# Performance work log

Measured on AMD Instinct MI355X. Metric: run time of the kernel, lower is better.

## Reference

```python
import jax, jax.numpy as jnp
import numpy as np

B, T, N_EMBD, HEAD_SIZE = 64, 512, 384, 64


def setup_inputs() -> dict:
    key = jax.random.key(0)
    k1, k2, k3, k4 = jax.random.split(key, 4)
    x = jax.random.normal(k1, (B, T, N_EMBD), dtype=jnp.float32)
    scale = 1.0 / np.sqrt(N_EMBD)
    Wq = jax.random.normal(k2, (N_EMBD, HEAD_SIZE), dtype=jnp.float32) * scale
    Wk = jax.random.normal(k3, (N_EMBD, HEAD_SIZE), dtype=jnp.float32) * scale
    Wv = jax.random.normal(k4, (N_EMBD, HEAD_SIZE), dtype=jnp.float32) * scale
    return {"x": x, "Wq": Wq, "Wk": Wk, "Wv": Wv}


def reference(x, Wq, Wk, Wv):
    # Single-head causal self-attention (dropout = identity / eval mode).
    q = jnp.einsum('btc,ch->bth', x, Wq)  # [B,T,H]
    k = jnp.einsum('btc,ch->bth', x, Wk)
    v = jnp.einsum('btc,ch->bth', x, Wv)
    scale = q.shape[-1] ** -0.5
    scores = jnp.einsum('bth,bsh->bts', q, k) * scale  # [B,T,T]
    Tlen = x.shape[1]
    causal = jnp.tril(jnp.ones((Tlen, Tlen), dtype=bool))
    scores = jnp.where(causal, scores, -jnp.inf)
    weights = jax.nn.softmax(scores, axis=-1)
    out = jnp.einsum('bts,bsh->bth', weights, v)  # [B,T,H]
    return out
```

## Files before the change

kernel.cpp:

```cpp
#include <hip/hip_runtime.h>


typedef __bf16 bf16_t;
typedef __bf16 bf16x8 __attribute__((ext_vector_type(8)));
typedef __bf16 bf16x4 __attribute__((ext_vector_type(4)));
typedef float  f32x4  __attribute__((ext_vector_type(4)));

__device__ __forceinline__ bf16x8 ld_b128(const bf16_t* p) {
    return *reinterpret_cast<const bf16x8*>(p);
}

__device__ __forceinline__ void async_copy16(void* lds, const void* g) {
    __builtin_amdgcn_global_load_lds(
        (const __attribute__((address_space(1))) unsigned int*)g,
        (__attribute__((address_space(3))) unsigned int*)lds,
        16, 0, 0);
}

__global__ __launch_bounds__(256) void wt_kernel(const float* __restrict__ Wq,
                                                 const float* __restrict__ Wk,
                                                 const float* __restrict__ Wv,
                                                 bf16_t* __restrict__ Wt) {
    int idx = blockIdx.x * 256 + threadIdx.x;
    int p = idx / (384 * 64);
    int r = idx - p * (384 * 64);
    int c = r >> 6;
    int h = r & 63;
    const float* W = (p == 0) ? Wq : (p == 1) ? Wk : Wv;
    Wt[p * 24576 + h * 384 + c] = (bf16_t)W[c * 64 + h];
}

__global__ __launch_bounds__(256, 2) void qkv_kernel(const float* __restrict__ x,
                                                     const bf16_t* __restrict__ Wt,
                                                     bf16_t* __restrict__ Q,
                                                     bf16_t* __restrict__ K,
                                                     bf16_t* __restrict__ Vt) {
    const int tid  = threadIdx.x;
    const int wave = tid >> 6, lane = tid & 63;
    const int quad = lane >> 4, l16 = lane & 15;
    const int rowbase = blockIdx.x * 64;
    const int batch   = rowbase >> 9;

    __shared__ alignas(16) float xs[2][64 * 128];

    bf16x8 Bf[3][12];
    #pragma unroll
    for (int nt = 0; nt < 3; ++nt) {
        int col  = wave * 48 + nt * 16 + l16;
        int proj = col >> 6, h = col & 63;
        const bf16_t* wp = Wt + proj * 24576 + h * 384 + quad * 8;
        #pragma unroll
        for (int kk = 0; kk < 12; ++kk) Bf[nt][kk] = ld_b128(wp + kk * 32);
    }

    auto stage = [&](int buf, int c) {
        const float* src = x + rowbase * 384 + c * 128;
        #pragma unroll
        for (int i = 0; i < 8; ++i) {
            int g   = wave * 512 + i * 64 + lane;
            int row = g >> 5, gc = g & 31;
            int gs  = (gc & 24) | ((gc ^ row) & 7);
            async_copy16(&xs[buf][(wave * 512 + i * 64) * 4],
                         src + row * 384 + gs * 4);
        }
    };

    f32x4 acc[4][3];
    #pragma unroll
    for (int rt = 0; rt < 4; ++rt)
        #pragma unroll
        for (int nt = 0; nt < 3; ++nt) acc[rt][nt] = (f32x4){0.f, 0.f, 0.f, 0.f};

    stage(0, 0);
    for (int c = 0; c < 3; ++c) {
        int buf = c & 1;
        __syncthreads();
        if (c < 2) stage(1 - buf, c + 1);
        #pragma unroll
        for (int rt = 0; rt < 4; ++rt) {
            int row = rt * 16 + l16;
            const float* xr = &xs[buf][row * 128];
            #pragma unroll
            for (int kk = 0; kk < 4; ++kk) {
                int G0 = kk * 8 + quad * 2;
                int g0 = (G0 & 24) | ((G0 ^ row) & 7);
                int g1 = ((G0 + 1) & 24) | (((G0 + 1) ^ row) & 7);
                f32x4 a0 = *reinterpret_cast<const f32x4*>(xr + g0 * 4);
                f32x4 a1 = *reinterpret_cast<const f32x4*>(xr + g1 * 4);
                bf16x8 a = {(bf16_t)a0[0], (bf16_t)a0[1], (bf16_t)a0[2], (bf16_t)a0[3],
                            (bf16_t)a1[0], (bf16_t)a1[1], (bf16_t)a1[2], (bf16_t)a1[3]};
                #pragma unroll
                for (int nt = 0; nt < 3; ++nt)
                    acc[rt][nt] = __builtin_amdgcn_mfma_f32_16x16x32_bf16(
                        a, Bf[nt][c * 4 + kk], acc[rt][nt], 0, 0, 0);
            }
        }
    }

    #pragma unroll
    for (int rt = 0; rt < 4; ++rt) {
        #pragma unroll
        for (int nt = 0; nt < 3; ++nt) {
            int col  = wave * 48 + nt * 16 + l16;
            int proj = col >> 6, h = col & 63;
            int trow = rowbase + rt * 16 + quad * 4;
            if (proj == 0) {
                #pragma unroll
                for (int r = 0; r < 4; ++r) Q[(trow + r) * 64 + h] = (bf16_t)acc[rt][nt][r];
            } else if (proj == 1) {
                #pragma unroll
                for (int r = 0; r < 4; ++r) K[(trow + r) * 64 + h] = (bf16_t)acc[rt][nt][r];
            } else {
                bf16x4 v = {(bf16_t)acc[rt][nt][0], (bf16_t)acc[rt][nt][1],
                            (bf16_t)acc[rt][nt][2], (bf16_t)acc[rt][nt][3]};
                *reinterpret_cast<bf16x4*>(Vt + batch * 32768 + h * 512 + (trow & 511)) = v;
            }
        }
    }
}

__global__ __launch_bounds__(256, 2) void attn_kernel(const bf16_t* __restrict__ Q,
                                                      const bf16_t* __restrict__ K,
                                                      const bf16_t* __restrict__ Vt,
                                                      float* __restrict__ out) {
    const int tid  = threadIdx.x;
    const int wave = tid >> 6, lane = tid & 63;
    const int quad = lane >> 4, l16 = lane & 15;
    const int b    = blockIdx.x >> 3;
    const int j    = blockIdx.x & 7;
    const int rbase = j * 64 + wave * 16;
    const int rowq  = rbase + quad * 4;

    __shared__ alignas(16) bf16_t Kt[2][64 * 64];
    __shared__ alignas(16) bf16_t Vtt[2][64 * 64];
    __shared__ alignas(16) bf16_t Pl[4][16 * 64];

    const bf16_t* Kb = K  + b * 32768;
    const bf16_t* Vb = Vt + b * 32768;

    const bf16_t* qptr = Q + (b * 512 + rbase + l16) * 64 + quad * 8;
    bf16x8 aq0 = ld_b128(qptr);
    bf16x8 aq1 = ld_b128(qptr + 32);

    f32x4 acc_o[4];
    #pragma unroll
    for (int nt = 0; nt < 4; ++nt) acc_o[nt] = (f32x4){0.f, 0.f, 0.f, 0.f};
    float l_lane[4] = {0.f, 0.f, 0.f, 0.f};

    auto stage = [&](int buf, int kb) {
        #pragma unroll
        for (int i = 0; i < 2; ++i) {
            int rr = wave * 16 + i * 8 + (lane >> 3);
            int g  = (lane & 7) ^ (rr & 7);
            async_copy16(&Kt[buf][(wave * 16 + i * 8) * 64],
                         Kb + (kb + rr) * 64 + g * 8);
            async_copy16(&Vtt[buf][(wave * 16 + i * 8) * 64],
                         Vb + rr * 512 + kb + g * 8);
        }
    };

    stage(0, 0);
    for (int kt = 0; kt <= j; ++kt) {
        int buf = kt & 1;
        __syncthreads();
        if (kt < j) stage(1 - buf, (kt + 1) * 64);
        int kb = kt * 64;
        bool last = (kt == j);

        float s[4][4];
        #pragma unroll
        for (int nt = 0; nt < 4; ++nt) {
            int tk = nt * 16 + l16;
            f32x4 c = (f32x4){0.f, 0.f, 0.f, 0.f};
            bf16x8 bk0 = ld_b128(&Kt[buf][tk * 64 + (((0 + quad) ^ (tk & 7)) << 3)]);
            c = __builtin_amdgcn_mfma_f32_16x16x32_bf16(aq0, bk0, c, 0, 0, 0);
            bf16x8 bk1 = ld_b128(&Kt[buf][tk * 64 + (((4 + quad) ^ (tk & 7)) << 3)]);
            c = __builtin_amdgcn_mfma_f32_16x16x32_bf16(aq1, bk1, c, 0, 0, 0);
            #pragma unroll
            for (int r = 0; r < 4; ++r) s[nt][r] = c[r];
        }
        if (last) {
            #pragma unroll
            for (int nt = 0; nt < 4; ++nt)
                #pragma unroll
                for (int r = 0; r < 4; ++r)
                    if (kb + nt * 16 + l16 > rowq + r) s[nt][r] = -__builtin_inff();
        }

        bf16_t* pw = &Pl[wave][0];
        #pragma unroll
        for (int nt = 0; nt < 4; ++nt) {
            #pragma unroll
            for (int r = 0; r < 4; ++r) {
                float p = __expf(fmaf(s[nt][r], 0.125f, -20.0f));
                l_lane[r] += p;
                int rl  = quad * 4 + r;
                int col = nt * 16 + l16;
                pw[rl * 64 + (((col >> 3) ^ (rl & 7)) << 3) + (col & 7)] = (bf16_t)p;
            }
        }
        bf16x8 ap0 = ld_b128(&pw[l16 * 64 + (((0 + quad) ^ (l16 & 7)) << 3)]);
        bf16x8 ap1 = ld_b128(&pw[l16 * 64 + (((4 + quad) ^ (l16 & 7)) << 3)]);
        #pragma unroll
        for (int nth = 0; nth < 4; ++nth) {
            int h = nth * 16 + l16;
            bf16x8 bv0 = ld_b128(&Vtt[buf][h * 64 + (((0 + quad) ^ (h & 7)) << 3)]);
            acc_o[nth] = __builtin_amdgcn_mfma_f32_16x16x32_bf16(ap0, bv0, acc_o[nth], 0, 0, 0);
            bf16x8 bv1 = ld_b128(&Vtt[buf][h * 64 + (((4 + quad) ^ (h & 7)) << 3)]);
            acc_o[nth] = __builtin_amdgcn_mfma_f32_16x16x32_bf16(ap1, bv1, acc_o[nth], 0, 0, 0);
        }
    }

    #pragma unroll
    for (int r = 0; r < 4; ++r) {
        float l = l_lane[r];
        #pragma unroll
        for (int xm = 1; xm < 16; xm <<= 1) l += __shfl_xor(l, xm, 64);
        l_lane[r] = l;
    }

    #pragma unroll
    for (int nth = 0; nth < 4; ++nth) {
        #pragma unroll
        for (int r = 0; r < 4; ++r) {
            out[(b * 512 + rowq + r) * 64 + nth * 16 + l16] =
                acc_o[nth][r] / l_lane[r];
        }
    }
}

extern "C" void kernel_launch(void* const* d_in, const int* in_sizes, int n_in,
                              void* d_out, int out_size, void* d_ws, size_t ws_size,
                              hipStream_t stream) {
    const float* x  = (const float*)d_in[0];
    const float* Wq = (const float*)d_in[1];
    const float* Wk = (const float*)d_in[2];
    const float* Wv = (const float*)d_in[3];

    char* ws = (char*)d_ws;
    bf16_t* Wt = (bf16_t*)(ws);
    bf16_t* Q  = (bf16_t*)(ws + 147456);
    bf16_t* K  = (bf16_t*)(ws + 147456 + 4194304);
    bf16_t* Vt = (bf16_t*)(ws + 147456 + 8388608);

    wt_kernel<<<dim3(288), dim3(256), 0, stream>>>(Wq, Wk, Wv, Wt);
    qkv_kernel<<<dim3(512), dim3(256), 0, stream>>>(x, Wt, Q, K, Vt);
    attn_kernel<<<dim3(512), dim3(256), 0, stream>>>(Q, K, Vt, (float*)d_out);
}
```

Before: 117.0 us.

## Fuse weight cast, QKV projection and attention into one persistent kernel with grid barriers

Merges the three kernel launches into a single 512-block kernel that uses atomic-counter grid barriers between the weight-transpose, QKV projection and attention phases. Q stays in shared memory instead of going through global memory, and blocks are remapped so each one handles the attention rows it projected, with causal work balanced across the launch order. This removes launch gaps and the Q round trip. In exchange it adds a memset launch and two device-wide spin barriers, and it relies on all 512 blocks being co-resident, which could deadlock if occupancy is lower than assumed.

```diff
diff --git a/kernel.cpp b/kernel.cpp
--- a/kernel.cpp
+++ b/kernel.cpp
@@ -17,214 +17,230 @@
         16, 0, 0);
 }
 
-__global__ __launch_bounds__(256) void wt_kernel(const float* __restrict__ Wq,
-                                                 const float* __restrict__ Wk,
-                                                 const float* __restrict__ Wv,
-                                                 bf16_t* __restrict__ Wt) {
-    int idx = blockIdx.x * 256 + threadIdx.x;
-    int p = idx / (384 * 64);
-    int r = idx - p * (384 * 64);
-    int c = r >> 6;
-    int h = r & 63;
-    const float* W = (p == 0) ? Wq : (p == 1) ? Wk : Wv;
-    Wt[p * 24576 + h * 384 + c] = (bf16_t)W[c * 64 + h];
-}
-
-__global__ __launch_bounds__(256, 2) void qkv_kernel(const float* __restrict__ x,
-                                                     const bf16_t* __restrict__ Wt,
-                                                     bf16_t* __restrict__ Q,
-                                                     bf16_t* __restrict__ K,
-                                                     bf16_t* __restrict__ Vt) {
+__device__ __forceinline__ void grid_barrier(unsigned* ctr, unsigned target) {
+    __syncthreads();
+    if (threadIdx.x == 0) {
+        __threadfence();
+        __hip_atomic_fetch_add(ctr, 1u, __ATOMIC_ACQ_REL, __HIP_MEMORY_SCOPE_AGENT);
+        while (__hip_atomic_load(ctr, __ATOMIC_ACQUIRE, __HIP_MEMORY_SCOPE_AGENT) < target)
+            __builtin_amdgcn_s_sleep(2);
+        __threadfence();
+    }
+    __syncthreads();
+}
+
+__global__ __launch_bounds__(256, 2)
+void head_fused(const float* __restrict__ x,
+                const float* __restrict__ Wq,
+                const float* __restrict__ Wk,
+                const float* __restrict__ Wv,
+                bf16_t* __restrict__ Wt,
+                bf16_t* __restrict__ K,
+                bf16_t* __restrict__ Vt,
+                float*  __restrict__ out,
+                unsigned* __restrict__ ctr) {
     const int tid  = threadIdx.x;
     const int wave = tid >> 6, lane = tid & 63;
     const int quad = lane >> 4, l16 = lane & 15;
-    const int rowbase = blockIdx.x * 64;
-    const int batch   = rowbase >> 9;
-
-    __shared__ alignas(16) float xs[2][64 * 128];
-
-    bf16x8 Bf[3][12];
-    #pragma unroll
-    for (int nt = 0; nt < 3; ++nt) {
-        int col  = wave * 48 + nt * 16 + l16;
-        int proj = col >> 6, h = col & 63;
-        const bf16_t* wp = Wt + proj * 24576 + h * 384 + quad * 8;
-        #pragma unroll
-        for (int kk = 0; kk < 12; ++kk) Bf[nt][kk] = ld_b128(wp + kk * 32);
-    }
-
-    auto stage = [&](int buf, int c) {
+    const int g    = blockIdx.x;
+
+    const int bb = g & 63;
+    const int jj = (g < 256) ? (g >> 6) : (7 - ((g - 256) >> 6));
+    const int rowbase = bb * 512 + jj * 64;
+
+    __shared__ union {
+        struct { float  xs[2][64 * 128];
+                 bf16_t Qs[64][72]; } p1;
+        struct { bf16_t Kt[2][64 * 64];
+                 bf16_t Vtt[2][64 * 64];
+                 bf16_t Pl[4][16 * 64]; } p2;
+    } sm;
+
+    auto stage_x = [&](int buf, int c) {
         const float* src = x + rowbase * 384 + c * 128;
         #pragma unroll
         for (int i = 0; i < 8; ++i) {
-            int g   = wave * 512 + i * 64 + lane;
-            int row = g >> 5, gc = g & 31;
+            int gr  = wave * 512 + i * 64 + lane;
+            int row = gr >> 5, gc = gr & 31;
             int gs  = (gc & 24) | ((gc ^ row) & 7);
-            async_copy16(&xs[buf][(wave * 512 + i * 64) * 4],
+            async_copy16(&sm.p1.xs[buf][(wave * 512 + i * 64) * 4],
                          src + row * 384 + gs * 4);
         }
     };
-
-    f32x4 acc[4][3];
-    #pragma unroll
-    for (int rt = 0; rt < 4; ++rt)
-        #pragma unroll
-        for (int nt = 0; nt < 3; ++nt) acc[rt][nt] = (f32x4){0.f, 0.f, 0.f, 0.f};
-
-    stage(0, 0);
-    for (int c = 0; c < 3; ++c) {
-        int buf = c & 1;
-        __syncthreads();
-        if (c < 2) stage(1 - buf, c + 1);
-        #pragma unroll
-        for (int rt = 0; rt < 4; ++rt) {
-            int row = rt * 16 + l16;
-            const float* xr = &xs[buf][row * 128];
-            #pragma unroll
-            for (int kk = 0; kk < 4; ++kk) {
-                int G0 = kk * 8 + quad * 2;
-                int g0 = (G0 & 24) | ((G0 ^ row) & 7);
-                int g1 = ((G0 + 1) & 24) | (((G0 + 1) ^ row) & 7);
-                f32x4 a0 = *reinterpret_cast<const f32x4*>(xr + g0 * 4);
-                f32x4 a1 = *reinterpret_cast<const f32x4*>(xr + g1 * 4);
-                bf16x8 a = {(bf16_t)a0[0], (bf16_t)a0[1], (bf16_t)a0[2], (bf16_t)a0[3],
-                            (bf16_t)a1[0], (bf16_t)a1[1], (bf16_t)a1[2], (bf16_t)a1[3]};
-                #pragma unroll
-                for (int nt = 0; nt < 3; ++nt)
-                    acc[rt][nt] = __builtin_amdgcn_mfma_f32_16x16x32_bf16(
-                        a, Bf[nt][c * 4 + kk], acc[rt][nt], 0, 0, 0);
-            }
-        }
-    }
-
-    #pragma unroll
-    for (int rt = 0; rt < 4; ++rt) {
+    stage_x(0, 0);
+
+    {
+        int idx = g * 256 + tid;
+        if (idx < 3 * 384 * 64) {
+            int p = idx / (384 * 64);
+            int r = idx - p * (384 * 64);
+            int c = r >> 6, h = r & 63;
+            const float* W = (p == 0) ? Wq : (p == 1) ? Wk : Wv;
+            Wt[p * 24576 + h * 384 + c] = (bf16_t)W[c * 64 + h];
+        }
+    }
+    grid_barrier(ctr, 512);
+
+    {
+        bf16x8 Bf[3][12];
         #pragma unroll
         for (int nt = 0; nt < 3; ++nt) {
             int col  = wave * 48 + nt * 16 + l16;
             int proj = col >> 6, h = col & 63;
-            int trow = rowbase + rt * 16 + quad * 4;
-            if (proj == 0) {
-                #pragma unroll
-                for (int r = 0; r < 4; ++r) Q[(trow + r) * 64 + h] = (bf16_t)acc[rt][nt][r];
-            } else if (proj == 1) {
-                #pragma unroll
-                for (int r = 0; r < 4; ++r) K[(trow + r) * 64 + h] = (bf16_t)acc[rt][nt][r];
-            } else {
-                bf16x4 v = {(bf16_t)acc[rt][nt][0], (bf16_t)acc[rt][nt][1],
-                            (bf16_t)acc[rt][nt][2], (bf16_t)acc[rt][nt][3]};
-                *reinterpret_cast<bf16x4*>(Vt + batch * 32768 + h * 512 + (trow & 511)) = v;
-            }
-        }
-    }
-}
-
-__global__ __launch_bounds__(256, 2) void attn_kernel(const bf16_t* __restrict__ Q,
-                                                      const bf16_t* __restrict__ K,
-                                                      const bf16_t* __restrict__ Vt,
-                                                      float* __restrict__ out) {
-    const int tid  = threadIdx.x;
-    const int wave = tid >> 6, lane = tid & 63;
-    const int quad = lane >> 4, l16 = lane & 15;
-    const int b    = blockIdx.x >> 3;
-    const int j    = blockIdx.x & 7;
-    const int rbase = j * 64 + wave * 16;
-    const int rowq  = rbase + quad * 4;
-
-    __shared__ alignas(16) bf16_t Kt[2][64 * 64];
-    __shared__ alignas(16) bf16_t Vtt[2][64 * 64];
-    __shared__ alignas(16) bf16_t Pl[4][16 * 64];
-
-    const bf16_t* Kb = K  + b * 32768;
-    const bf16_t* Vb = Vt + b * 32768;
-
-    const bf16_t* qptr = Q + (b * 512 + rbase + l16) * 64 + quad * 8;
-    bf16x8 aq0 = ld_b128(qptr);
-    bf16x8 aq1 = ld_b128(qptr + 32);
-
-    f32x4 acc_o[4];
-    #pragma unroll
-    for (int nt = 0; nt < 4; ++nt) acc_o[nt] = (f32x4){0.f, 0.f, 0.f, 0.f};
-    float l_lane[4] = {0.f, 0.f, 0.f, 0.f};
-
-    auto stage = [&](int buf, int kb) {
-        #pragma unroll
-        for (int i = 0; i < 2; ++i) {
-            int rr = wave * 16 + i * 8 + (lane >> 3);
-            int g  = (lane & 7) ^ (rr & 7);
-            async_copy16(&Kt[buf][(wave * 16 + i * 8) * 64],
-                         Kb + (kb + rr) * 64 + g * 8);
-            async_copy16(&Vtt[buf][(wave * 16 + i * 8) * 64],
-                         Vb + rr * 512 + kb + g * 8);
-        }
-    };
-
-    stage(0, 0);
-    for (int kt = 0; kt <= j; ++kt) {
-        int buf = kt & 1;
+            const bf16_t* wp = Wt + proj * 24576 + h * 384 + quad * 8;
+            #pragma unroll
+            for (int kk = 0; kk < 12; ++kk) Bf[nt][kk] = ld_b128(wp + kk * 32);
+        }
+
+        f32x4 acc[4][3];
+        #pragma unroll
+        for (int rt = 0; rt < 4; ++rt)
+            #pragma unroll
+            for (int nt = 0; nt < 3; ++nt) acc[rt][nt] = (f32x4){0.f, 0.f, 0.f, 0.f};
+
+        for (int c = 0; c < 3; ++c) {
+            int buf = c & 1;
+            __syncthreads();
+            if (c < 2) stage_x(1 - buf, c + 1);
+            #pragma unroll
+            for (int rt = 0; rt < 4; ++rt) {
+                int row = rt * 16 + l16;
+                const float* xr = &sm.p1.xs[buf][row * 128];
+                #pragma unroll
+                for (int kk = 0; kk < 4; ++kk) {
+                    int G0 = kk * 8 + quad * 2;
+                    int g0 = (G0 & 24) | ((G0 ^ row) & 7);
+                    int g1 = ((G0 + 1) & 24) | (((G0 + 1) ^ row) & 7);
+                    f32x4 a0 = *reinterpret_cast<const f32x4*>(xr + g0 * 4);
+                    f32x4 a1 = *reinterpret_cast<const f32x4*>(xr + g1 * 4);
+                    bf16x8 a = {(bf16_t)a0[0], (bf16_t)a0[1], (bf16_t)a0[2], (bf16_t)a0[3],
+                                (bf16_t)a1[0], (bf16_t)a1[1], (bf16_t)a1[2], (bf16_t)a1[3]};
+                    #pragma unroll
+                    for (int nt = 0; nt < 3; ++nt)
+                        acc[rt][nt] = __builtin_amdgcn_mfma_f32_16x16x32_bf16(
+                            a, Bf[nt][c * 4 + kk], acc[rt][nt], 0, 0, 0);
+                }
+            }
+        }
         __syncthreads();
-        if (kt < j) stage(1 - buf, (kt + 1) * 64);
-        int kb = kt * 64;
-        bool last = (kt == j);
-
-        float s[4][4];
-        #pragma unroll
-        for (int nt = 0; nt < 4; ++nt) {
-            int tk = nt * 16 + l16;
-            f32x4 c = (f32x4){0.f, 0.f, 0.f, 0.f};
-            bf16x8 bk0 = ld_b128(&Kt[buf][tk * 64 + (((0 + quad) ^ (tk & 7)) << 3)]);
-            c = __builtin_amdgcn_mfma_f32_16x16x32_bf16(aq0, bk0, c, 0, 0, 0);
-            bf16x8 bk1 = ld_b128(&Kt[buf][tk * 64 + (((4 + quad) ^ (tk & 7)) << 3)]);
-            c = __builtin_amdgcn_mfma_f32_16x16x32_bf16(aq1, bk1, c, 0, 0, 0);
-            #pragma unroll
-            for (int r = 0; r < 4; ++r) s[nt][r] = c[r];
-        }
-        if (last) {
-            #pragma unroll
-            for (int nt = 0; nt < 4; ++nt)
-                #pragma unroll
-                for (int r = 0; r < 4; ++r)
-                    if (kb + nt * 16 + l16 > rowq + r) s[nt][r] = -__builtin_inff();
-        }
-
-        bf16_t* pw = &Pl[wave][0];
-        #pragma unroll
-        for (int nt = 0; nt < 4; ++nt) {
+
+        #pragma unroll
+        for (int rt = 0; rt < 4; ++rt) {
+            #pragma unroll
+            for (int nt = 0; nt < 3; ++nt) {
+                int col  = wave * 48 + nt * 16 + l16;
+                int proj = col >> 6, h = col & 63;
+                int rloc = rt * 16 + quad * 4;
+                int trow = rowbase + rloc;
+                if (proj == 0) {
+                    #pragma unroll
+                    for (int r = 0; r < 4; ++r) sm.p1.Qs[rloc + r][h] = (bf16_t)acc[rt][nt][r];
+                } else if (proj == 1) {
+                    #pragma unroll
+                    for (int r = 0; r < 4; ++r) K[(trow + r) * 64 + h] = (bf16_t)acc[rt][nt][r];
+                } else {
+                    bf16x4 v = {(bf16_t)acc[rt][nt][0], (bf16_t)acc[rt][nt][1],
+                                (bf16_t)acc[rt][nt][2], (bf16_t)acc[rt][nt][3]};
+                    *reinterpret_cast<bf16x4*>(Vt + bb * 32768 + h * 512 + (trow & 511)) = v;
+                }
+            }
+        }
+    }
+    grid_barrier(ctr, 1024);
+
+    {
+        const int rbase = jj * 64 + wave * 16;
+        const int rowq  = rbase + quad * 4;
+        const bf16_t* Kb = K  + bb * 32768;
+        const bf16_t* Vb = Vt + bb * 32768;
+
+        const bf16_t* qrow = &sm.p1.Qs[wave * 16 + l16][quad * 8];
+        bf16x8 aq0 = *reinterpret_cast<const bf16x8*>(qrow);
+        bf16x8 aq1 = *reinterpret_cast<const bf16x8*>(qrow + 32);
+
+        f32x4 acc_o[4];
+        #pragma unroll
+        for (int nt = 0; nt < 4; ++nt) acc_o[nt] = (f32x4){0.f, 0.f, 0.f, 0.f};
+        float l_lane[4] = {0.f, 0.f, 0.f, 0.f};
+
+        auto stage_kv = [&](int buf, int kb) {
+            #pragma unroll
+            for (int i = 0; i < 2; ++i) {
+                int rr = wave * 16 + i * 8 + (lane >> 3);
+                int gg = (lane & 7) ^ (rr & 7);
+                async_copy16(&sm.p2.Kt[buf][(wave * 16 + i * 8) * 64],
+                             Kb + (kb + rr) * 64 + gg * 8);
+                async_copy16(&sm.p2.Vtt[buf][(wave * 16 + i * 8) * 64],
+                             Vb + rr * 512 + kb + gg * 8);
+            }
+        };
+
+        stage_kv(0, 0);
+        for (int kt = 0; kt <= jj; ++kt) {
+            int buf = kt & 1;
+            __syncthreads();
+            if (kt < jj) stage_kv(1 - buf, (kt + 1) * 64);
+            int kb = kt * 64;
+            bool last = (kt == jj);
+
+            float s[4][4];
+            #pragma unroll
+            for (int nt = 0; nt < 4; ++nt) {
+                int tk = nt * 16 + l16;
+                f32x4 c = (f32x4){0.f, 0.f, 0.f, 0.f};
+                bf16x8 bk0 = ld_b128(&sm.p2.Kt[buf][tk * 64 + (((0 + quad) ^ (tk & 7)) << 3)]);
+                c = __builtin_amdgcn_mfma_f32_16x16x32_bf16(aq0, bk0, c, 0, 0, 0);
+                bf16x8 bk1 = ld_b128(&sm.p2.Kt[buf][tk * 64 + (((4 + quad) ^ (tk & 7)) << 3)]);
+                c = __builtin_amdgcn_mfma_f32_16x16x32_bf16(aq1, bk1, c, 0, 0, 0);
+                #pragma unroll
+                for (int r = 0; r < 4; ++r) s[nt][r] = c[r];
+            }
+            if (last) {
+                #pragma unroll
+                for (int nt = 0; nt < 4; ++nt)
+                    #pragma unroll
+                    for (int r = 0; r < 4; ++r)
+                        if (kb + nt * 16 + l16 > rowq + r) s[nt][r] = -__builtin_inff();
+            }
+
+            bf16_t* pw = &sm.p2.Pl[wave][0];
+            #pragma unroll
+            for (int nt = 0; nt < 4; ++nt) {
+                #pragma unroll
+                for (int r = 0; r < 4; ++r) {
+                    float p = __expf(fmaf(s[nt][r], 0.125f, -20.0f));
+                    l_lane[r] += p;
+                    int rl  = quad * 4 + r;
+                    int col = nt * 16 + l16;
+                    pw[rl * 64 + (((col >> 3) ^ (rl & 7)) << 3) + (col & 7)] = (bf16_t)p;
+                }
+            }
+            bf16x8 ap0 = ld_b128(&pw[l16 * 64 + (((0 + quad) ^ (l16 & 7)) << 3)]);
+            bf16x8 ap1 = ld_b128(&pw[l16 * 64 + (((4 + quad) ^ (l16 & 7)) << 3)]);
+            #pragma unroll
+            for (int nth = 0; nth < 4; ++nth) {
+                int h = nth * 16 + l16;
+                bf16x8 bv0 = ld_b128(&sm.p2.Vtt[buf][h * 64 + (((0 + quad) ^ (h & 7)) << 3)]);
+                acc_o[nth] = __builtin_amdgcn_mfma_f32_16x16x32_bf16(ap0, bv0, acc_o[nth], 0, 0, 0);
+                bf16x8 bv1 = ld_b128(&sm.p2.Vtt[buf][h * 64 + (((4 + quad) ^ (h & 7)) << 3)]);
+                acc_o[nth] = __builtin_amdgcn_mfma_f32_16x16x32_bf16(ap1, bv1, acc_o[nth], 0, 0, 0);
+            }
+        }
+
+        #pragma unroll
+        for (int r = 0; r < 4; ++r) {
+            float l = l_lane[r];
+            #pragma unroll
+            for (int xm = 1; xm < 16; xm <<= 1) l += __shfl_xor(l, xm, 64);
+            l_lane[r] = l;
+        }
+        #pragma unroll
+        for (int nth = 0; nth < 4; ++nth) {
             #pragma unroll
             for (int r = 0; r < 4; ++r) {
-                float p = __expf(fmaf(s[nt][r], 0.125f, -20.0f));
-                l_lane[r] += p;
-                int rl  = quad * 4 + r;
-                int col = nt * 16 + l16;
-                pw[rl * 64 + (((col >> 3) ^ (rl & 7)) << 3) + (col & 7)] = (bf16_t)p;
-            }
-        }
-        bf16x8 ap0 = ld_b128(&pw[l16 * 64 + (((0 + quad) ^ (l16 & 7)) << 3)]);
-        bf16x8 ap1 = ld_b128(&pw[l16 * 64 + (((4 + quad) ^ (l16 & 7)) << 3)]);
-        #pragma unroll
-        for (int nth = 0; nth < 4; ++nth) {
-            int h = nth * 16 + l16;
-            bf16x8 bv0 = ld_b128(&Vtt[buf][h * 64 + (((0 + quad) ^ (h & 7)) << 3)]);
-            acc_o[nth] = __builtin_amdgcn_mfma_f32_16x16x32_bf16(ap0, bv0, acc_o[nth], 0, 0, 0);
-            bf16x8 bv1 = ld_b128(&Vtt[buf][h * 64 + (((4 + quad) ^ (h & 7)) << 3)]);
-            acc_o[nth] = __builtin_amdgcn_mfma_f32_16x16x32_bf16(ap1, bv1, acc_o[nth], 0, 0, 0);
-        }
-    }
-
-    #pragma unroll
-    for (int r = 0; r < 4; ++r) {
-        float l = l_lane[r];
-        #pragma unroll
-        for (int xm = 1; xm < 16; xm <<= 1) l += __shfl_xor(l, xm, 64);
-        l_lane[r] = l;
-    }
-
-    #pragma unroll
-    for (int nth = 0; nth < 4; ++nth) {
-        #pragma unroll
-        for (int r = 0; r < 4; ++r) {
-            out[(b * 512 + rowq + r) * 64 + nth * 16 + l16] =
-                acc_o[nth][r] / l_lane[r];
+                out[(bb * 512 + rowq + r) * 64 + nth * 16 + l16] =
+                    acc_o[nth][r] / l_lane[r];
+            }
         }
     }
 }
@@ -238,12 +254,12 @@
     const float* Wv = (const float*)d_in[3];
 
     char* ws = (char*)d_ws;
-    bf16_t* Wt = (bf16_t*)(ws);
-    bf16_t* Q  = (bf16_t*)(ws + 147456);
-    bf16_t* K  = (bf16_t*)(ws + 147456 + 4194304);
-    bf16_t* Vt = (bf16_t*)(ws + 147456 + 8388608);
-
-    wt_kernel<<<dim3(288), dim3(256), 0, stream>>>(Wq, Wk, Wv, Wt);
-    qkv_kernel<<<dim3(512), dim3(256), 0, stream>>>(x, Wt, Q, K, Vt);
-    attn_kernel<<<dim3(512), dim3(256), 0, stream>>>(Q, K, Vt, (float*)d_out);
-}
+    unsigned* ctr = (unsigned*)ws;
+    bf16_t* Wt = (bf16_t*)(ws + 512);
+    bf16_t* K  = (bf16_t*)(ws + 512 + 147456);
+    bf16_t* Vt = (bf16_t*)(ws + 512 + 147456 + 4194304);
+
+    hipMemsetAsync(ctr, 0, 64, stream);
+    head_fused<<<dim3(512), dim3(256), 0, stream>>>(x, Wq, Wk, Wv, Wt, K, Vt,
+                                                    (float*)d_out, ctr);
+}
```

Result: slower. 257.1 us (+119.8%).

## Halve QKV tile rows with single-shot staging and reorder attention blocks by causal length

Applied to the files above, without the earlier changes.

The QKV projection kernel now gives each block 32 rows instead of 64 and loads the whole 32x384 fp32 x tile into LDS in one asynchronous pass. This replaces the double-buffered three-chunk loop and doubles the grid to 1024 blocks, which is meant to improve occupancy and load balance. The attention kernel remaps block indices so that the heaviest causal query tiles (large j) are scheduled first, interleaved across batches, to reduce tail imbalance. The cost is that x loads no longer overlap with the MFMA work, and each block reloads the full weight fragments from global memory for half as many rows.

```diff
diff --git a/kernel.cpp b/kernel.cpp
--- a/kernel.cpp
+++ b/kernel.cpp
@@ -38,10 +38,19 @@
     const int tid  = threadIdx.x;
     const int wave = tid >> 6, lane = tid & 63;
     const int quad = lane >> 4, l16 = lane & 15;
-    const int rowbase = blockIdx.x * 64;
+    const int rowbase = blockIdx.x * 32;
     const int batch   = rowbase >> 9;
 
-    __shared__ alignas(16) float xs[2][64 * 128];
+    __shared__ alignas(16) float xs[32 * 384];
+
+    const float* src = x + rowbase * 384;
+    #pragma unroll
+    for (int i = 0; i < 12; ++i) {
+        int g   = i * 256 + tid;
+        int row = g / 96, gc = g - row * 96;
+        int gs  = (gc & ~7) | ((gc ^ row) & 7);
+        async_copy16(&xs[(i * 256 + wave * 64) * 4], src + row * 384 + gs * 4);
+    }
 
     bf16x8 Bf[3][12];
     #pragma unroll
@@ -53,52 +62,36 @@
         for (int kk = 0; kk < 12; ++kk) Bf[nt][kk] = ld_b128(wp + kk * 32);
     }
 
-    auto stage = [&](int buf, int c) {
-        const float* src = x + rowbase * 384 + c * 128;
-        #pragma unroll
-        for (int i = 0; i < 8; ++i) {
-            int g   = wave * 512 + i * 64 + lane;
-            int row = g >> 5, gc = g & 31;
-            int gs  = (gc & 24) | ((gc ^ row) & 7);
-            async_copy16(&xs[buf][(wave * 512 + i * 64) * 4],
-                         src + row * 384 + gs * 4);
-        }
-    };
-
-    f32x4 acc[4][3];
-    #pragma unroll
-    for (int rt = 0; rt < 4; ++rt)
+    __syncthreads();
+
+    f32x4 acc[2][3];
+    #pragma unroll
+    for (int rt = 0; rt < 2; ++rt)
         #pragma unroll
         for (int nt = 0; nt < 3; ++nt) acc[rt][nt] = (f32x4){0.f, 0.f, 0.f, 0.f};
 
-    stage(0, 0);
-    for (int c = 0; c < 3; ++c) {
-        int buf = c & 1;
-        __syncthreads();
-        if (c < 2) stage(1 - buf, c + 1);
-        #pragma unroll
-        for (int rt = 0; rt < 4; ++rt) {
+    #pragma unroll
+    for (int kk = 0; kk < 12; ++kk) {
+        #pragma unroll
+        for (int rt = 0; rt < 2; ++rt) {
             int row = rt * 16 + l16;
-            const float* xr = &xs[buf][row * 128];
-            #pragma unroll
-            for (int kk = 0; kk < 4; ++kk) {
-                int G0 = kk * 8 + quad * 2;
-                int g0 = (G0 & 24) | ((G0 ^ row) & 7);
-                int g1 = ((G0 + 1) & 24) | (((G0 + 1) ^ row) & 7);
-                f32x4 a0 = *reinterpret_cast<const f32x4*>(xr + g0 * 4);
-                f32x4 a1 = *reinterpret_cast<const f32x4*>(xr + g1 * 4);
-                bf16x8 a = {(bf16_t)a0[0], (bf16_t)a0[1], (bf16_t)a0[2], (bf16_t)a0[3],
-                            (bf16_t)a1[0], (bf16_t)a1[1], (bf16_t)a1[2], (bf16_t)a1[3]};
-                #pragma unroll
-                for (int nt = 0; nt < 3; ++nt)
-                    acc[rt][nt] = __builtin_amdgcn_mfma_f32_16x16x32_bf16(
-                        a, Bf[nt][c * 4 + kk], acc[rt][nt], 0, 0, 0);
-            }
-        }
-    }
-
-    #pragma unroll
-    for (int rt = 0; rt < 4; ++rt) {
+            const float* xr = &xs[row * 384];
+            int G0 = kk * 8 + quad * 2;
+            int g0 = (G0 & ~7) | ((G0 ^ row) & 7);
+            int g1 = ((G0 + 1) & ~7) | (((G0 + 1) ^ row) & 7);
+            f32x4 a0 = *reinterpret_cast<const f32x4*>(xr + g0 * 4);
+            f32x4 a1 = *reinterpret_cast<const f32x4*>(xr + g1 * 4);
+            bf16x8 a = {(bf16_t)a0[0], (bf16_t)a0[1], (bf16_t)a0[2], (bf16_t)a0[3],
+                        (bf16_t)a1[0], (bf16_t)a1[1], (bf16_t)a1[2], (bf16_t)a1[3]};
+            #pragma unroll
+            for (int nt = 0; nt < 3; ++nt)
+                acc[rt][nt] = __builtin_amdgcn_mfma_f32_16x16x32_bf16(
+                    a, Bf[nt][kk], acc[rt][nt], 0, 0, 0);
+        }
+    }
+
+    #pragma unroll
+    for (int rt = 0; rt < 2; ++rt) {
         #pragma unroll
         for (int nt = 0; nt < 3; ++nt) {
             int col  = wave * 48 + nt * 16 + l16;
@@ -126,8 +119,9 @@
     const int tid  = threadIdx.x;
     const int wave = tid >> 6, lane = tid & 63;
     const int quad = lane >> 4, l16 = lane & 15;
-    const int b    = blockIdx.x >> 3;
-    const int j    = blockIdx.x & 7;
+    const int g    = blockIdx.x;
+    const int b    = g & 63;
+    const int j    = (g < 256) ? (g >> 6) : (7 - ((g - 256) >> 6));
     const int rbase = j * 64 + wave * 16;
     const int rowq  = rbase + quad * 4;
 
@@ -151,11 +145,11 @@
         #pragma unroll
         for (int i = 0; i < 2; ++i) {
             int rr = wave * 16 + i * 8 + (lane >> 3);
-            int g  = (lane & 7) ^ (rr & 7);
+            int gg = (lane & 7) ^ (rr & 7);
             async_copy16(&Kt[buf][(wave * 16 + i * 8) * 64],
-                         Kb + (kb + rr) * 64 + g * 8);
+                         Kb + (kb + rr) * 64 + gg * 8);
             async_copy16(&Vtt[buf][(wave * 16 + i * 8) * 64],
-                         Vb + rr * 512 + kb + g * 8);
+                         Vb + rr * 512 + kb + gg * 8);
         }
     };
 
@@ -244,6 +238,6 @@
     bf16_t* Vt = (bf16_t*)(ws + 147456 + 8388608);
 
     wt_kernel<<<dim3(288), dim3(256), 0, stream>>>(Wq, Wk, Wv, Wt);
-    qkv_kernel<<<dim3(512), dim3(256), 0, stream>>>(x, Wt, Q, K, Vt);
+    qkv_kernel<<<dim3(1024), dim3(256), 0, stream>>>(x, Wt, Q, K, Vt);
     attn_kernel<<<dim3(512), dim3(256), 0, stream>>>(Q, K, Vt, (float*)d_out);
 }
```

After: 119.5 us. 1.02x slower.
